# Optimization experiments

Measured on AMD Instinct MI355X. Metric: run time of the kernel, lower is better.

## Reference

```python
import jax, jax.numpy as jnp
import numpy as np


def setup_inputs() -> dict:
    key = jax.random.key(0)
    ks = jax.random.split(key, 14)
    B, Ld, Lq, D = 64, 512, 128, 512
    d_node = jax.random.normal(ks[0], (B, Ld, D), jnp.float32)
    q_node = jax.random.normal(ks[1], (B, Lq, D), jnp.float32)
    qq_graph = jax.random.randint(ks[2], (B, Lq, Lq), 0, 2, jnp.int32)
    dq_graph = jax.random.randint(ks[3], (B, Ld, Lq), 0, 2, jnp.int32)
    dd_graph = jax.random.randint(ks[4], (B, Ld, Ld), 0, 2, jnp.int32)
    qd_graph = jax.random.randint(ks[5], (B, Lq, Ld), 0, 2, jnp.int32)
    s = 0.02
    W_nw = jax.random.normal(ks[6], (1, D), jnp.float32) * s
    b_nw = jnp.zeros((1,), jnp.float32)
    W_self = jax.random.normal(ks[7], (D, D), jnp.float32) * s
    b_self = jnp.zeros((D,), jnp.float32)
    W_dd = jax.random.normal(ks[8], (D, D), jnp.float32) * s
    W_qq = jax.random.normal(ks[9], (D, D), jnp.float32) * s
    W_dq = jax.random.normal(ks[10], (D, D), jnp.float32) * s
    W_qd = jax.random.normal(ks[11], (D, D), jnp.float32) * s
    return {"d_node": d_node, "q_node": q_node, "qq_graph": qq_graph,
            "dq_graph": dq_graph, "dd_graph": dd_graph, "qd_graph": qd_graph,
            "W_nw": W_nw, "b_nw": b_nw, "W_self": W_self, "b_self": b_self,
            "W_dd": W_dd, "W_qq": W_qq, "W_dq": W_dq, "W_qd": W_qd,
            "iteration_steps": 2}


def reference(d_node, q_node, qq_graph, dq_graph, dd_graph, qd_graph,
              W_nw, b_nw, W_self, b_self, W_dd, W_qq, W_dq, W_qd,
              iteration_steps):
    dd = dd_graph.astype(jnp.float32)
    dq = dq_graph.astype(jnp.float32)
    qq = qq_graph.astype(jnp.float32)
    qd = qd_graph.astype(jnp.float32)

    # neighbor counts, clamped to 1 where a node has no neighbors
    d_nb = dd.sum(-1) + dq.sum(-1)              # [B, Ld]
    d_nb = jnp.where(d_nb >= 1.0, d_nb, 1.0)
    q_nb = qq.sum(-1) + qd.sum(-1)              # [B, Lq]
    q_nb = jnp.where(q_nb >= 1.0, q_nb, 1.0)

    all_d_w, all_q_w = [], []
    for _ in range(iteration_steps):
        d_w = jax.nn.sigmoid(jnp.einsum('bld,od->blo', d_node, W_nw) + b_nw)[..., 0]  # [B, Ld]
        q_w = jax.nn.sigmoid(jnp.einsum('bld,od->blo', q_node, W_nw) + b_nw)[..., 0]  # [B, Lq]
        all_d_w.append(d_w)
        all_q_w.append(q_w)

        self_d = jnp.einsum('bld,od->blo', d_node, W_self) + b_self
        self_q = jnp.einsum('bld,od->blo', q_node, W_self) + b_self
        dd_info = jnp.einsum('bld,od->blo', d_node, W_dd)
        qd_info = jnp.einsum('bld,od->blo', d_node, W_qd)
        qq_info = jnp.einsum('bld,od->blo', q_node, W_qq)
        dq_info = jnp.einsum('bld,od->blo', q_node, W_dq)

        # masked weights: graph is 0/1, so replace_masked_values(., graph, 0) == graph * weight
        dd_msg = jnp.einsum('bij,bjd->bid', dd * d_w[:, None, :], dd_info)  # [B,Ld,D]
        qd_msg = jnp.einsum('bij,bjd->bid', qd * d_w[:, None, :], qd_info)  # [B,Lq,D]
        qq_msg = jnp.einsum('bij,bjd->bid', qq * q_w[:, None, :], qq_info)  # [B,Lq,D]
        dq_msg = jnp.einsum('bij,bjd->bid', dq * q_w[:, None, :], dq_info)  # [B,Ld,D]

        agg_q = (qq_msg + qd_msg) / q_nb[..., None]
        agg_d = (dd_msg + dq_msg) / d_nb[..., None]
        d_node = jax.nn.relu(self_d + agg_d)
        q_node = jax.nn.relu(self_q + agg_q)

    all_d_w = jnp.stack(all_d_w, axis=1)  # [B, steps, Ld]
    all_q_w = jnp.stack(all_q_w, axis=1)  # [B, steps, Lq]
    return (d_node, q_node, all_d_w, all_q_w)
```

## Files before the change

### kernel.cpp

```cpp
#include <hip/hip_runtime.h>
#include <cstdint>
#include <cstddef>

typedef _Float16 h16;
typedef __attribute__((ext_vector_type(8))) _Float16 h16x8;
typedef __attribute__((ext_vector_type(4))) _Float16 h16x4;
typedef __attribute__((ext_vector_type(4))) float f32x4;

constexpr int B_ = 64, LD = 512, LQ = 128, DIM = 512, STEPS = 2;
constexpr int MD = B_ * LD;
constexpr int MQ = B_ * LQ;
constexpr int KST = LD + LQ;
constexpr int KAGG = KST + DIM;

#define ASYNC16(gp, lp)                                                          \
  __builtin_amdgcn_global_load_lds(                                              \
      (const __attribute__((address_space(1))) unsigned int*)(gp),               \
      (__attribute__((address_space(3))) unsigned int*)(lp), 16, 0, 0)

struct Src {
  const h16* p0; int s0; long bstr0;
  const h16* p1; int s1; long bstr1;
  int ksplit;
};

template <class Epi>
__device__ __forceinline__ void gemm_body(int b, long tileM, long tileN,
                                          Src sa, Src sb, int K,
                                          const Epi& epi, h16* lds) {
  const int tid = threadIdx.x;
  const int lane = tid & 63;
  const int wv = tid >> 6;
  const int wm = (wv >> 1) * 64, wn = (wv & 1) * 64;
  const int quad = lane >> 4, l16 = lane & 15;

  const int r = tid >> 2;
  const int es = (r ^ (r >> 2)) & 3;
  const int kq = (tid & 3) ^ es;

  const h16* pa0 = sa.p0 + (size_t)b * sa.bstr0 + (tileM + r) * (long)sa.s0 + kq * 8;
  const h16* pa0h = pa0 + 64L * sa.s0;
  const h16* pa1 = sa.p1 + (size_t)b * sa.bstr1 + (tileM + r) * (long)sa.s1 + kq * 8 - sa.ksplit;
  const h16* pa1h = pa1 + 64L * sa.s1;
  const h16* pb0 = sb.p0 + (size_t)b * sb.bstr0 + (tileN + r) * (long)sb.s0 + kq * 8;
  const h16* pb0h = pb0 + 64L * sb.s0;
  const h16* pb1 = sb.p1 + (size_t)b * sb.bstr1 + (tileN + r) * (long)sb.s1 + kq * 8 - sb.ksplit;
  const h16* pb1h = pb1 + 64L * sb.s1;

  h16* const dA = &lds[tid * 8];
  h16* const dB = &lds[4096 + tid * 8];

  const int ef = (l16 ^ (l16 >> 2)) & 3;
  const h16* fA[4];
  const h16* fB[4];
#pragma unroll
  for (int t = 0; t < 4; t++) {
    const int rowA = wm + t * 16 + l16;
    const int rowB = wn + t * 16 + l16;
    fA[t] = &lds[(rowA * 4 + (quad ^ ef)) * 8];
    fB[t] = &lds[4096 + (rowB * 4 + (quad ^ ef)) * 8];
  }

  f32x4 acc[4][4] = {};
  const int T = K >> 5;

  auto dmaTile = [&](int t, int c) {
    const int k0 = t * 32;
    const int o = c * 8192;
    const bool fa = k0 < sa.ksplit;
    ASYNC16((fa ? pa0 : pa1) + k0, dA + o);
    ASYNC16((fa ? pa0h : pa1h) + k0, dA + o + 2048);
    const bool fb = k0 < sb.ksplit;
    ASYNC16((fb ? pb0 : pb1) + k0, dB + o);
    ASYNC16((fb ? pb0h : pb1h) + k0, dB + o + 2048);
  };
  auto mfma16 = [&](int off) {
    h16x8 af[4], bf[4];
#pragma unroll
    for (int i = 0; i < 4; i++) {
      af[i] = *(const h16x8*)(fA[i] + off);
      bf[i] = *(const h16x8*)(fB[i] + off);
    }
#pragma unroll
    for (int i = 0; i < 4; i++)
#pragma unroll
      for (int j = 0; j < 4; j++)
        acc[i][j] = __builtin_amdgcn_mfma_f32_16x16x32_f16(af[i], bf[j], acc[i][j], 0, 0, 0);
  };

  dmaTile(0, 0);

  for (int t = 0; t < T; t += 2) {
    __syncthreads();
    dmaTile(t + 1, 1);
    mfma16(0);
    __syncthreads();
    if (t + 2 < T) dmaTile(t + 2, 0);
    mfma16(8192);
  }

#pragma unroll
  for (int i = 0; i < 4; i++) {
#pragma unroll
    for (int j = 0; j < 4; j++) {
      const int gm0 = (int)tileM + wm + i * 16 + quad * 4;
      const int gn  = (int)tileN + wn + j * 16 + l16;
#pragma unroll
      for (int rr = 0; rr < 4; rr++) epi(b, gm0 + rr, gn, acc[i][j][rr]);
    }
  }
}

struct EpiDense {
  const float* w;
  h16* stackA;
  h16* stackB;
  int lnShift;
  int offA, offB;
  __device__ void operator()(int, int gm, int gn, float v) const {
    const int b = gn >> lnShift, l = gn & ((1 << lnShift) - 1);
    const h16 sv = (h16)(w[gn] * v);
    if (gm < 512)
      stackA[((size_t)b * 512 + gm) * 640 + offA + l] = sv;
    else
      stackB[((size_t)b * 512 + (gm - 512)) * 640 + offB + l] = sv;
  }
};
struct EpiAgg {
  const float* bias;
  float* out;
  h16* nodeNext;
  int rowsPerB;
  __device__ void operator()(int b, int gm, int gn, float v) const {
    const size_t row = (size_t)b * rowsPerB + gm;
    const float val = fmaxf(v + bias[gn], 0.f);
    if (out) out[row * 512 + gn] = val;
    nodeNext[row * 512 + gn] = (h16)val;
  }
};

__global__ __launch_bounds__(256, 3) void k_dense(Src saD, Src sbD, EpiDense epiD,
                                                  Src saQ, Src sbQ, EpiDense epiQ) {
  __shared__ __align__(16) h16 lds[2 * 2 * 4096];
  const int g = blockIdx.x;
  const int x = g / 320;
  const int yy = g % 320;
  if (yy < 256)
    gemm_body(0, (long)x * 128, (long)yy * 128, saD, sbD, 512, epiD, lds);
  else
    gemm_body(0, (long)x * 128, (long)(yy - 256) * 128, saQ, sbQ, 512, epiQ, lds);
}

__global__ __launch_bounds__(256, 3) void k_agg(Src saD, Src sbD, EpiAgg epiD,
                                                Src saQ, Src sbQ, EpiAgg epiQ) {
  __shared__ __align__(16) h16 lds[2 * 2 * 4096];
  const int g = blockIdx.x;
  const int b = g & 63;
  const int inner = g >> 6;
  if (inner < 16)
    gemm_body(b, (long)(inner >> 2) * 128, (long)(inner & 3) * 128, saD, sbD, KAGG, epiD, lds);
  else
    gemm_body(b, 0L, (long)(inner - 16) * 128, saQ, sbQ, KAGG, epiQ, lds);
}

__global__ __launch_bounds__(256) void k_convert(const float* __restrict__ dn,
                                                 const float* __restrict__ qn,
                                                 h16* __restrict__ dnb,
                                                 h16* __restrict__ qnb) {
  const size_t i4 = ((size_t)blockIdx.x * 256 + threadIdx.x) * 4;
  constexpr size_t TD = (size_t)MD * DIM;
  const float* src; h16* dst; size_t idx;
  if (i4 < TD) { src = dn; dst = dnb; idx = i4; }
  else         { src = qn; dst = qnb; idx = i4 - TD; }
  const float4 v = *(const float4*)&src[idx];
  h16x4 o; o.x = (h16)v.x; o.y = (h16)v.y; o.z = (h16)v.z; o.w = (h16)v.w;
  *(h16x4*)&dst[idx] = o;
}

__global__ __launch_bounds__(256) void k_wcat(const float* __restrict__ Wself,
                                              const float* __restrict__ Wdd,
                                              const float* __restrict__ Wqd,
                                              const float* __restrict__ Wqq,
                                              const float* __restrict__ Wdq,
                                              h16* __restrict__ catD,
                                              h16* __restrict__ catQ) {
  const int i = blockIdx.x * 256 + threadIdx.x;
  float vD, vQ;
  if (i < 512 * 512)       { vD = Wself[i];            vQ = vD; }
  else if (i < 1024 * 512) { vD = Wdd[i - 512 * 512];  vQ = Wqq[i - 512 * 512]; }
  else                     { vD = Wqd[i - 1024 * 512]; vQ = Wdq[i - 1024 * 512]; }
  catD[i] = (h16)vD; catQ[i] = (h16)vQ;
}

__global__ __launch_bounds__(256) void k_maskD(const int* __restrict__ dd,
                                               const int* __restrict__ dq,
                                               h16* __restrict__ maskD) {
  const int row = blockIdx.x * 4 + (threadIdx.x >> 6);
  const int lane = threadIdx.x & 63;
  const int* pdd = dd + (size_t)row * 512;
  const int* pdq = dq + (size_t)row * 128;
  h16* pm = maskD + (size_t)row * 640;
  float vals[10];
  float s = 0.f;
#pragma unroll
  for (int t = 0; t < 10; t++) {
    const int j = lane + t * 64;
    const float v = (float)((j < 512) ? pdd[j] : pdq[j - 512]);
    vals[t] = v; s += v;
  }
  for (int m = 32; m; m >>= 1) s += __shfl_xor(s, m);
  const float inv = 1.f / fmaxf(s, 1.f);
#pragma unroll
  for (int t = 0; t < 10; t++) pm[lane + t * 64] = (h16)(vals[t] * inv);
}

__global__ __launch_bounds__(256) void k_maskQ(const int* __restrict__ qq,
                                               const int* __restrict__ qd,
                                               h16* __restrict__ maskQ) {
  const int row = blockIdx.x * 4 + (threadIdx.x >> 6);
  const int lane = threadIdx.x & 63;
  const int* pqq = qq + (size_t)row * 128;
  const int* pqd = qd + (size_t)row * 512;
  h16* pm = maskQ + (size_t)row * 640;
  float vals[10];
  float s = 0.f;
#pragma unroll
  for (int t = 0; t < 10; t++) {
    const int j = lane + t * 64;
    const float v = (float)((j < 128) ? pqq[j] : pqd[j - 128]);
    vals[t] = v; s += v;
  }
  for (int m = 32; m; m >>= 1) s += __shfl_xor(s, m);
  const float inv = 1.f / fmaxf(s, 1.f);
#pragma unroll
  for (int t = 0; t < 10; t++) pm[lane + t * 64] = (h16)(vals[t] * inv);
}

__global__ __launch_bounds__(256) void k_w(const h16* __restrict__ dnb,
                                           const h16* __restrict__ qnb,
                                           const float* __restrict__ Wnw,
                                           const float* __restrict__ bnw,
                                           float* __restrict__ d_w,
                                           float* __restrict__ q_w,
                                           float* __restrict__ adw,
                                           float* __restrict__ aqw, int it) {
  const int row = blockIdx.x * 4 + (threadIdx.x >> 6);
  const int lane = threadIdx.x & 63;
  const bool isD = row < MD;
  const h16* node = isD ? dnb + (size_t)row * 512 : qnb + (size_t)(row - MD) * 512;
  const h16x8 v = *(const h16x8*)&node[lane * 8];
  const float4 w0 = *(const float4*)&Wnw[lane * 8];
  const float4 w1 = *(const float4*)&Wnw[lane * 8 + 4];
  float s = (float)v[0] * w0.x + (float)v[1] * w0.y + (float)v[2] * w0.z +
            (float)v[3] * w0.w + (float)v[4] * w1.x + (float)v[5] * w1.y +
            (float)v[6] * w1.z + (float)v[7] * w1.w;
  for (int m = 32; m; m >>= 1) s += __shfl_xor(s, m);
  if (lane == 0) {
    const float w = 1.f / (1.f + expf(-(s + bnw[0])));
    if (isD) {
      d_w[row] = w;
      adw[((size_t)(row >> 9) * STEPS + it) * 512 + (row & 511)] = w;
    } else {
      const int rq = row - MD;
      q_w[rq] = w;
      aqw[((size_t)(rq >> 7) * STEPS + it) * 128 + (rq & 127)] = w;
    }
  }
}

extern "C" void kernel_launch(void* const* d_in, const int* in_sizes, int n_in,
                              void* d_out, int out_size, void* d_ws, size_t ws_size,
                              hipStream_t stream) {
  (void)in_sizes; (void)n_in; (void)out_size; (void)ws_size;

  const float* d_node = (const float*)d_in[0];
  const float* q_node = (const float*)d_in[1];
  const int*   qq     = (const int*)d_in[2];
  const int*   dq     = (const int*)d_in[3];
  const int*   dd     = (const int*)d_in[4];
  const int*   qd     = (const int*)d_in[5];
  const float* W_nw   = (const float*)d_in[6];
  const float* b_nw   = (const float*)d_in[7];
  const float* W_self = (const float*)d_in[8];
  const float* b_self = (const float*)d_in[9];
  const float* W_dd   = (const float*)d_in[10];
  const float* W_qq   = (const float*)d_in[11];
  const float* W_dq   = (const float*)d_in[12];
  const float* W_qd   = (const float*)d_in[13];

  float* outd = (float*)d_out;
  float* outq = outd + (size_t)MD * DIM;
  float* adw  = outq + (size_t)MQ * DIM;
  float* aqw  = adw + (size_t)B_ * STEPS * LD;

  char* p = (char*)d_ws;
  auto alloc = [&](size_t bytes) { char* r = p; p += (bytes + 255) & ~(size_t)255; return r; };
  h16* dnode[2], *qnode[2];
  dnode[0] = (h16*)alloc((size_t)MD * DIM * 2);
  dnode[1] = (h16*)alloc((size_t)MD * DIM * 2);
  qnode[0] = (h16*)alloc((size_t)MQ * DIM * 2);
  qnode[1] = (h16*)alloc((size_t)MQ * DIM * 2);
  h16* catD    = (h16*)alloc((size_t)1536 * 512 * 2);
  h16* catQ    = (h16*)alloc((size_t)1536 * 512 * 2);
  h16* maskD   = (h16*)alloc((size_t)B_ * LD * KST * 2);
  h16* maskQ   = (h16*)alloc((size_t)B_ * LQ * KST * 2);
  h16* stackDT = (h16*)alloc((size_t)B_ * 512 * KST * 2);
  h16* stackQT = (h16*)alloc((size_t)B_ * 512 * KST * 2);
  float* d_wb  = (float*)alloc((size_t)MD * 4);
  float* q_wb  = (float*)alloc((size_t)MQ * 4);

  k_convert<<<dim3((MD * DIM + MQ * DIM) / 4 / 256), 256, 0, stream>>>(d_node, q_node, dnode[0], qnode[0]);
  k_wcat<<<dim3(1536 * 512 / 256), 256, 0, stream>>>(W_self, W_dd, W_qd, W_qq, W_dq, catD, catQ);
  k_maskD<<<dim3(MD / 4), 256, 0, stream>>>(dd, dq, maskD);
  k_maskQ<<<dim3(MQ / 4), 256, 0, stream>>>(qq, qd, maskQ);

  for (int it = 0; it < STEPS; it++) {
    const bool last = (it == STEPS - 1);
    h16* ncur_d = dnode[it & 1];
    h16* nnext_d = dnode[(it & 1) ^ 1];
    h16* ncur_q = qnode[it & 1];
    h16* nnext_q = qnode[(it & 1) ^ 1];

    k_w<<<dim3((MD + MQ) / 4), 256, 0, stream>>>(ncur_d, ncur_q, W_nw, b_nw, d_wb, q_wb, adw, aqw, it);

    {
      Src saD{catD + 512 * 512, 512, 0, catD + 512 * 512, 512, 0, 512};
      Src sbD{ncur_d, 512, 0, ncur_d, 512, 0, 512};
      Src saQ{catQ + 512 * 512, 512, 0, catQ + 512 * 512, 512, 0, 512};
      Src sbQ{ncur_q, 512, 0, ncur_q, 512, 0, 512};
      k_dense<<<dim3(2560), 256, 0, stream>>>(
          saD, sbD, EpiDense{d_wb, stackDT, stackQT, 9, 0, 128},
          saQ, sbQ, EpiDense{q_wb, stackQT, stackDT, 7, 0, 512});
    }
    {
      Src saD{maskD, 640, (long)LD * KST, ncur_d, 512, (long)LD * DIM, KST};
      Src sbD{stackDT, 640, (long)512 * KST, catD, 512, 0, KST};
      Src saQ{maskQ, 640, (long)LQ * KST, ncur_q, 512, (long)LQ * DIM, KST};
      Src sbQ{stackQT, 640, (long)512 * KST, catQ, 512, 0, KST};
      k_agg<<<dim3(1280), 256, 0, stream>>>(
          saD, sbD, EpiAgg{b_self, last ? outd : nullptr, nnext_d, 512},
          saQ, sbQ, EpiAgg{b_self, last ? outq : nullptr, nnext_q, 128});
    }
  }
}
```

Baseline: 568.9 us.

## Enlarge GEMM tiles to 256x128 with templated per-wave M size

Makes the shared GEMM body a template on wave M-tiles, so dense and D-side aggregation GEMMs use 256x128 block tiles (8x4 MFMA accumulators per wave), while the Q aggregation uses 128x128. The goal is more operand reuse per LDS load and fewer blocks and global loads, which halves grid sizes. In exchange it doubles accumulator registers and enlarges LDS, cutting occupancy (launch bounds 3 to 2) and possibly leaving fewer blocks than needed to fill all CUs.

```diff
diff --git a/kernel.cpp b/kernel.cpp
--- a/kernel.cpp
+++ b/kernel.cpp
@@ -24,65 +24,72 @@
   int ksplit;
 };
 
-template <class Epi>
+template <int WM, class Epi>
 __device__ __forceinline__ void gemm_body(int b, long tileM, long tileN,
                                           Src sa, Src sb, int K,
                                           const Epi& epi, h16* lds) {
+  constexpr int BM = WM * 32;
+  constexpr int AS = BM / 64;
+  constexpr int AE = BM * 32;
+  constexpr int BUFE = AE + 4096;
+
   const int tid = threadIdx.x;
   const int lane = tid & 63;
   const int wv = tid >> 6;
-  const int wm = (wv >> 1) * 64, wn = (wv & 1) * 64;
+  const int wi = wv >> 1, wj = wv & 1;
   const int quad = lane >> 4, l16 = lane & 15;
 
   const int r = tid >> 2;
   const int es = (r ^ (r >> 2)) & 3;
   const int kq = (tid & 3) ^ es;
 
-  const h16* pa0 = sa.p0 + (size_t)b * sa.bstr0 + (tileM + r) * (long)sa.s0 + kq * 8;
-  const h16* pa0h = pa0 + 64L * sa.s0;
-  const h16* pa1 = sa.p1 + (size_t)b * sa.bstr1 + (tileM + r) * (long)sa.s1 + kq * 8 - sa.ksplit;
-  const h16* pa1h = pa1 + 64L * sa.s1;
-  const h16* pb0 = sb.p0 + (size_t)b * sb.bstr0 + (tileN + r) * (long)sb.s0 + kq * 8;
-  const h16* pb0h = pb0 + 64L * sb.s0;
-  const h16* pb1 = sb.p1 + (size_t)b * sb.bstr1 + (tileN + r) * (long)sb.s1 + kq * 8 - sb.ksplit;
-  const h16* pb1h = pb1 + 64L * sb.s1;
-
-  h16* const dA = &lds[tid * 8];
-  h16* const dB = &lds[4096 + tid * 8];
+  const h16* pa[2][AS];
+  const h16* pb[2][2];
+#pragma unroll
+  for (int s = 0; s < AS; s++) {
+    pa[0][s] = sa.p0 + (size_t)b * sa.bstr0 + (tileM + r + 64 * s) * (long)sa.s0 + kq * 8;
+    pa[1][s] = sa.p1 + (size_t)b * sa.bstr1 + (tileM + r + 64 * s) * (long)sa.s1 + kq * 8 - sa.ksplit;
+  }
+#pragma unroll
+  for (int s = 0; s < 2; s++) {
+    pb[0][s] = sb.p0 + (size_t)b * sb.bstr0 + (tileN + r + 64 * s) * (long)sb.s0 + kq * 8;
+    pb[1][s] = sb.p1 + (size_t)b * sb.bstr1 + (tileN + r + 64 * s) * (long)sb.s1 + kq * 8 - sb.ksplit;
+  }
 
   const int ef = (l16 ^ (l16 >> 2)) & 3;
-  const h16* fA[4];
-  const h16* fB[4];
-#pragma unroll
-  for (int t = 0; t < 4; t++) {
-    const int rowA = wm + t * 16 + l16;
-    const int rowB = wn + t * 16 + l16;
-    fA[t] = &lds[(rowA * 4 + (quad ^ ef)) * 8];
-    fB[t] = &lds[4096 + (rowB * 4 + (quad ^ ef)) * 8];
-  }
-
-  f32x4 acc[4][4] = {};
+  int offA[WM], offB[4];
+#pragma unroll
+  for (int i = 0; i < WM; i++) {
+    const int row = wi * WM * 16 + i * 16 + l16;
+    offA[i] = (row * 4 + (quad ^ ef)) * 8;
+  }
+#pragma unroll
+  for (int j = 0; j < 4; j++) {
+    const int row = wj * 64 + j * 16 + l16;
+    offB[j] = AE + (row * 4 + (quad ^ ef)) * 8;
+  }
+
+  f32x4 acc[WM][4] = {};
   const int T = K >> 5;
 
   auto dmaTile = [&](int t, int c) {
     const int k0 = t * 32;
-    const int o = c * 8192;
-    const bool fa = k0 < sa.ksplit;
-    ASYNC16((fa ? pa0 : pa1) + k0, dA + o);
-    ASYNC16((fa ? pa0h : pa1h) + k0, dA + o + 2048);
-    const bool fb = k0 < sb.ksplit;
-    ASYNC16((fb ? pb0 : pb1) + k0, dB + o);
-    ASYNC16((fb ? pb0h : pb1h) + k0, dB + o + 2048);
+    h16* base = lds + c * BUFE + tid * 8;
+    const int sel = (k0 >= sa.ksplit);
+#pragma unroll
+    for (int s = 0; s < AS; s++) ASYNC16(pa[sel][s] + k0, base + s * 2048);
+    const int selb = (k0 >= sb.ksplit);
+#pragma unroll
+    for (int s = 0; s < 2; s++) ASYNC16(pb[selb][s] + k0, base + AE + s * 2048);
   };
-  auto mfma16 = [&](int off) {
-    h16x8 af[4], bf[4];
-#pragma unroll
-    for (int i = 0; i < 4; i++) {
-      af[i] = *(const h16x8*)(fA[i] + off);
-      bf[i] = *(const h16x8*)(fB[i] + off);
-    }
-#pragma unroll
-    for (int i = 0; i < 4; i++)
+  auto mfmaStep = [&](int off) {
+    h16x8 af[WM], bf[4];
+#pragma unroll
+    for (int i = 0; i < WM; i++) af[i] = *(const h16x8*)(lds + off + offA[i]);
+#pragma unroll
+    for (int j = 0; j < 4; j++) bf[j] = *(const h16x8*)(lds + off + offB[j]);
+#pragma unroll
+    for (int i = 0; i < WM; i++)
 #pragma unroll
       for (int j = 0; j < 4; j++)
         acc[i][j] = __builtin_amdgcn_mfma_f32_16x16x32_f16(af[i], bf[j], acc[i][j], 0, 0, 0);
@@ -93,18 +100,18 @@
   for (int t = 0; t < T; t += 2) {
     __syncthreads();
     dmaTile(t + 1, 1);
-    mfma16(0);
+    mfmaStep(0);
     __syncthreads();
     if (t + 2 < T) dmaTile(t + 2, 0);
-    mfma16(8192);
-  }
-
-#pragma unroll
-  for (int i = 0; i < 4; i++) {
+    mfmaStep(BUFE);
+  }
+
+#pragma unroll
+  for (int i = 0; i < WM; i++) {
 #pragma unroll
     for (int j = 0; j < 4; j++) {
-      const int gm0 = (int)tileM + wm + i * 16 + quad * 4;
-      const int gn  = (int)tileN + wn + j * 16 + l16;
+      const int gm0 = (int)tileM + wi * WM * 16 + i * 16 + quad * 4;
+      const int gn  = (int)tileN + wj * 64 + j * 16 + l16;
 #pragma unroll
       for (int rr = 0; rr < 4; rr++) epi(b, gm0 + rr, gn, acc[i][j][rr]);
     }
@@ -139,28 +146,28 @@
   }
 };
 
-__global__ __launch_bounds__(256, 3) void k_dense(Src saD, Src sbD, EpiDense epiD,
+__global__ __launch_bounds__(256, 2) void k_dense(Src saD, Src sbD, EpiDense epiD,
                                                   Src saQ, Src sbQ, EpiDense epiQ) {
-  __shared__ __align__(16) h16 lds[2 * 2 * 4096];
+  __shared__ __align__(16) h16 lds[2 * (256 * 32 + 128 * 32)];
   const int g = blockIdx.x;
   const int x = g / 320;
   const int yy = g % 320;
   if (yy < 256)
-    gemm_body(0, (long)x * 128, (long)yy * 128, saD, sbD, 512, epiD, lds);
+    gemm_body<8>(0, (long)x * 256, (long)yy * 128, saD, sbD, 512, epiD, lds);
   else
-    gemm_body(0, (long)x * 128, (long)(yy - 256) * 128, saQ, sbQ, 512, epiQ, lds);
-}
-
-__global__ __launch_bounds__(256, 3) void k_agg(Src saD, Src sbD, EpiAgg epiD,
+    gemm_body<8>(0, (long)x * 256, (long)(yy - 256) * 128, saQ, sbQ, 512, epiQ, lds);
+}
+
+__global__ __launch_bounds__(256, 2) void k_agg(Src saD, Src sbD, EpiAgg epiD,
                                                 Src saQ, Src sbQ, EpiAgg epiQ) {
-  __shared__ __align__(16) h16 lds[2 * 2 * 4096];
+  __shared__ __align__(16) h16 lds[2 * (256 * 32 + 128 * 32)];
   const int g = blockIdx.x;
   const int b = g & 63;
   const int inner = g >> 6;
-  if (inner < 16)
-    gemm_body(b, (long)(inner >> 2) * 128, (long)(inner & 3) * 128, saD, sbD, KAGG, epiD, lds);
+  if (inner < 8)
+    gemm_body<8>(b, (long)(inner >> 2) * 256, (long)(inner & 3) * 128, saD, sbD, KAGG, epiD, lds);
   else
-    gemm_body(b, 0L, (long)(inner - 16) * 128, saQ, sbQ, KAGG, epiQ, lds);
+    gemm_body<4>(b, 0L, (long)(inner - 8) * 128, saQ, sbQ, KAGG, epiQ, lds);
 }
 
 __global__ __launch_bounds__(256) void k_convert(const float* __restrict__ dn,
@@ -328,7 +335,7 @@
       Src sbD{ncur_d, 512, 0, ncur_d, 512, 0, 512};
       Src saQ{catQ + 512 * 512, 512, 0, catQ + 512 * 512, 512, 0, 512};
       Src sbQ{ncur_q, 512, 0, ncur_q, 512, 0, 512};
-      k_dense<<<dim3(2560), 256, 0, stream>>>(
+      k_dense<<<dim3(1280), 256, 0, stream>>>(
           saD, sbD, EpiDense{d_wb, stackDT, stackQT, 9, 0, 128},
           saQ, sbQ, EpiDense{q_wb, stackQT, stackDT, 7, 0, 512});
     }
@@ -337,7 +344,7 @@
       Src sbD{stackDT, 640, (long)512 * KST, catD, 512, 0, KST};
       Src saQ{maskQ, 640, (long)LQ * KST, ncur_q, 512, (long)LQ * DIM, KST};
       Src sbQ{stackQT, 640, (long)512 * KST, catQ, 512, 0, KST};
-      k_agg<<<dim3(1280), 256, 0, stream>>>(
+      k_agg<<<dim3(768), 256, 0, stream>>>(
           saD, sbD, EpiAgg{b_self, last ? outd : nullptr, nnext_d, 512},
           saQ, sbQ, EpiAgg{b_self, last ? outq : nullptr, nnext_q, 128});
     }
```

Result: faster. 544.7 us (-4.2%).
